# Optimization experiments

Hardware: AMD Instinct MI355X
Metric: run time of the kernel (lower is better)

The kernel has to match this reference:

```python
import jax, jax.numpy as jnp
import numpy as np
from jax import lax

DN = ('NCHW', 'OIHW', 'NCHW')

def conv(x, w, b):
    y = lax.conv_general_dilated(x, w, (1, 1), 'SAME', dimension_numbers=DN)
    return y + b[None, :, None, None]


def setup_inputs() -> dict:
    key = jax.random.key(0)
    ks = jax.random.split(key, 32)
    B, C, H, W = 16, 256, 40, 100
    dim, N, kd, ncls, mdim = 134, 4, 128, 2, 256
    inc = C + 2
    s = 0.05  # weight init scale
    def w(k, shape):
        return jax.random.normal(k, shape, jnp.float32) * s
    d = {}
    d['features'] = jax.random.normal(ks[0], (B, C, H, W), jnp.float32)
    d['iw0'] = w(ks[1], (dim, inc, 3, 3)); d['ib0'] = jnp.zeros((dim,), jnp.float32)
    d['iw1'] = w(ks[2], (dim, dim, 3, 3)); d['ib1'] = jnp.zeros((dim,), jnp.float32)
    d['iw2'] = w(ks[3], (dim, dim, 3, 3)); d['ib2'] = jnp.zeros((dim,), jnp.float32)
    d['iw3'] = w(ks[4], (dim, dim, 3, 3)); d['ib3'] = jnp.zeros((dim,), jnp.float32)
    d['iam_w'] = w(ks[5], (N, dim, 3, 3)); d['iam_b'] = jnp.zeros((N,), jnp.float32)
    d['cls_w'] = w(ks[6], (ncls, dim));    d['cls_b'] = jnp.zeros((ncls,), jnp.float32)
    d['mk_w'] = w(ks[7], (kd, dim));       d['mk_b'] = jnp.zeros((kd,), jnp.float32)
    d['mw0'] = w(ks[8], (mdim, inc, 3, 3));  d['mb0'] = jnp.zeros((mdim,), jnp.float32)
    d['mw1'] = w(ks[9], (mdim, mdim, 3, 3)); d['mb1'] = jnp.zeros((mdim,), jnp.float32)
    d['mw2'] = w(ks[10], (mdim, mdim, 3, 3)); d['mb2'] = jnp.zeros((mdim,), jnp.float32)
    d['mw3'] = w(ks[11], (mdim, mdim, 3, 3)); d['mb3'] = jnp.zeros((mdim,), jnp.float32)
    d['pw'] = w(ks[12], (kd, mdim, 1, 1));   d['pb'] = jnp.zeros((kd,), jnp.float32)
    return d


def reference(features, iw0, ib0, iw1, ib1, iw2, ib2, iw3, ib3, iam_w, iam_b,
              cls_w, cls_b, mk_w, mk_b, mw0, mb0, mw1, mb1, mw2, mb2, mw3, mb3, pw, pb):
    B, C, H, W = features.shape
    # coordinate channels in [-1, 1]
    y_loc = -1.0 + 2.0 * jnp.arange(H, dtype=jnp.float32) / (H - 1)
    x_loc = -1.0 + 2.0 * jnp.arange(W, dtype=jnp.float32) / (W - 1)
    yy, xx = jnp.meshgrid(y_loc, x_loc, indexing='ij')  # [H,W]
    coords = jnp.broadcast_to(jnp.stack([xx, yy], 0)[None], (B, 2, H, W))
    feat = jnp.concatenate([coords, features], axis=1)  # [B, C+2, H, W]

    # instance branch conv stack (258 -> 134, relu)
    f = jax.nn.relu(conv(feat, iw0, ib0))
    f = jax.nn.relu(conv(f, iw1, ib1))
    f = jax.nn.relu(conv(f, iw2, ib2))
    f = jax.nn.relu(conv(f, iw3, ib3))  # [B,134,H,W]

    params = jnp.transpose(f, (0, 2, 3, 1)).reshape(-1, 134)  # [B*H*W, 134]

    iam = conv(f, iam_w, iam_b)           # [B,N,H,W]
    iam_prob = jax.nn.sigmoid(iam)
    Bn, Ni = iam_prob.shape[:2]

    # seed extraction: per-map flat argmax (pos = r*W + c, label always 0 in original)
    pos = jnp.argmax(iam_prob.reshape(Bn * Ni, H * W), axis=-1)  # [B*N], values in [0, H*W)
    sel = params[pos]                     # gather rows (indexes batch-0 region, as in source)
    mask_params = sel[:, :67]
    reg_params = sel[:, 67:]

    # iam-weighted pooling
    ip = iam_prob.reshape(Bn, Ni, H * W)
    ip = ip / jnp.clip(ip.sum(-1, keepdims=True), 1e-6)
    inst = jnp.einsum('bnl,bcl->bnc', ip, f.reshape(Bn, 134, H * W))  # [B,N,134]

    pred_logits = inst @ cls_w.T + cls_b  # [B,N,2]
    pred_kernel = inst @ mk_w.T + mk_b    # [B,N,128]

    # mask branch (258 -> 256 x4 relu, then 1x1 projection to 128, no relu)
    m = jax.nn.relu(conv(feat, mw0, mb0))
    m = jax.nn.relu(conv(m, mw1, mb1))
    m = jax.nn.relu(conv(m, mw2, mb2))
    m = jax.nn.relu(conv(m, mw3, mb3))
    mf = conv(m, pw, pb)                  # [B,128,H,W]

    pred_masks = jnp.einsum('bnk,bkl->bnl', pred_kernel, mf.reshape(Bn, 128, H * W))
    pred_masks = pred_masks.reshape(Bn * Ni, H, W)
    pred_logits = pred_logits.reshape(Bn * Ni, -1)
    return pred_logits, mask_params, reg_params, pred_masks
```

## Files before the change

kernel.cpp:

```cpp
#include <hip/hip_runtime.h>
#include <hip/hip_bf16.h>
#include <math.h>

constexpr int HW = 4000;
constexpr int HP = 4284;
constexpr int HPAD = 4480;
constexpr int NPIXH = 16 * HP;

typedef short s16x8 __attribute__((ext_vector_type(8)));
typedef float f32x4 __attribute__((ext_vector_type(4)));
typedef unsigned short u16x4 __attribute__((ext_vector_type(4)));
typedef unsigned short u16;

__device__ __forceinline__ u16 f2bf(float f) {
    __hip_bfloat16 h = __float2bfloat16(f);
    u16 b; __builtin_memcpy(&b, &h, 2); return b;
}
__device__ __forceinline__ float bf2f(u16 b) {
    __hip_bfloat16 h; __builtin_memcpy(&h, &b, 2); return __bfloat162float(h);
}

__device__ __forceinline__ void gload_lds16(const void* g, void* l) {
    __builtin_amdgcn_global_load_lds(
        (const __attribute__((address_space(1))) void*)g,
        (__attribute__((address_space(3))) void*)l, 16, 0, 0);
}

__global__ __launch_bounds__(256) void repack_w(
    const float* __restrict__ W, u16* __restrict__ Wh, u16* __restrict__ Wl,
    int Cout, int Cin, int NRS, int nCh, int Npad, int do_lo)
{
    const int chunk = blockIdx.x * 256 + threadIdx.x;
    const int per = Npad * 4;
    const int total = NRS * nCh * per;
    if (chunk >= total) return;
    const int q = chunk % per;
    const int t2 = chunk / per;
    const int ch = t2 % nCh;
    const int rs = t2 / nCh;
    const int f = q >> 6, g = (q >> 4) & 3, rA = q & 15;
    const int n = f * 16 + rA;
    u16x4 hp[2], lp[2];
    #pragma unroll
    for (int j = 0; j < 8; ++j) {
        const int c = ch * 32 + g * 8 + j;
        const float v = (n < Cout && c < Cin) ? W[((size_t)n * Cin + c) * NRS + rs] : 0.f;
        const u16 hb = f2bf(v);
        hp[j >> 2][j & 3] = hb;
        lp[j >> 2][j & 3] = f2bf(v - bf2f(hb));
    }
    const size_t o = (size_t)chunk * 8;
    *(u16x4*)(Wh + o) = hp[0]; *(u16x4*)(Wh + o + 4) = hp[1];
    if (do_lo) { *(u16x4*)(Wl + o) = lp[0]; *(u16x4*)(Wl + o + 4) = lp[1]; }
}

__global__ __launch_bounds__(256) void prep_x0(
    const float* __restrict__ feat, u16* __restrict__ Xh, u16* __restrict__ Xl)
{
    const int p = blockIdx.x * 256 + threadIdx.x;
    if (p >= NPIXH) return;
    const int b = p / HP; const int rem = p - b * HP;
    const int hh = rem / 102, wp = rem - hh * 102;
    const bool halo = (hh == 0) | (hh == 41) | (wp == 0) | (wp == 101);
    const int h = hh - 1, w = wp - 1;
    const int hw = h * 100 + w;
    const float xw = -1.f + 2.f * (float)w / 99.f;
    const float yh = -1.f + 2.f * (float)h / 39.f;
    for (int g = 0; g < 36; ++g) {
        u16x4 hp[2], lp[2];
        #pragma unroll
        for (int j = 0; j < 8; ++j) {
            const int c = g * 8 + j;
            float v = 0.f;
            if (!halo) {
                if (c == 0) v = xw;
                else if (c == 1) v = yh;
                else if (c < 258) v = feat[((size_t)(b * 256 + (c - 2))) * HW + hw];
            }
            const u16 hb = f2bf(v);
            hp[j >> 2][j & 3] = hb;
            lp[j >> 2][j & 3] = f2bf(v - bf2f(hb));
        }
        const size_t o = ((size_t)(b * 36 + g) * HPAD + rem) * 8;
        *(u16x4*)(Xh + o) = hp[0]; *(u16x4*)(Xh + o + 4) = hp[1];
        *(u16x4*)(Xl + o) = lp[0]; *(u16x4*)(Xl + o + 4) = lp[1];
    }
}

__global__ __launch_bounds__(256) void zero_halo_pl(
    u16* __restrict__ pa, u16* __restrict__ pb, int nGa, int nGb)
{
    const int p = blockIdx.x * 256 + threadIdx.x;
    if (p >= NPIXH) return;
    const int b = p / HP; const int rem = p - b * HP;
    const int hh = rem / 102, wp = rem - hh * 102;
    if (!((hh == 0) | (hh == 41) | (wp == 0) | (wp == 101))) return;
    const u16x4 z = {0, 0, 0, 0};
    for (int g = 0; g < nGa; ++g) {
        const size_t o = ((size_t)(b * nGa + g) * HPAD + rem) * 8;
        *(u16x4*)(pa + o) = z; *(u16x4*)(pa + o + 4) = z;
    }
    if (pb)
        for (int g = 0; g < nGb; ++g) {
            const size_t o = ((size_t)(b * nGb + g) * HPAD + rem) * 8;
            *(u16x4*)(pb + o) = z; *(u16x4*)(pb + o + 4) = z;
        }
}

template <int SPLIT, int BN, int NRS, int OUTMODE, int NCH, int MINW>
__global__ __launch_bounds__(256, MINW) void conv_mfma(
    const u16* __restrict__ Xhi, const u16* __restrict__ Xlo,
    const u16* __restrict__ Whi, const u16* __restrict__ Wlo,
    const float* __restrict__ bias,
    u16* __restrict__ Yhi, u16* __restrict__ Ylo, float* __restrict__ Yf,
    int Npad, int Cout, int CoutStore, int nGout, int do_relu,
    int nN, int cpx)
{
    constexpr int FW = BN / 32;
    constexpr int PSTRIDE = 393;
    constexpr int NGIN = NCH * 4;
    constexpr int NPASS = (SPLIT == 3) ? 2 : 1;

    __shared__ u16 lsX[4 * PSTRIDE * 8];

    const int tid = threadIdx.x, lane = tid & 63, wid = tid >> 6;

    const int pb_ = blockIdx.x;
    const int s = (pb_ & 7) * cpx + (pb_ >> 3);
    const int nb = s % nN;
    const int mt = s / nN;
    const int mb = mt & 31, bimg = mt >> 5;
    const int off = mb * 128;
    const int n0 = nb * BN;
    const int h0 = off / 100, w0 = off - h0 * 100;
    const int pTL0 = h0 * 102 + w0;

    const int wn = (wid & 1) * (BN / 2);
    const int wm = (wid >> 1) * 64;
    const int gA = lane >> 4, rA = lane & 15;
    const int wq0 = ((n0 + wn) >> 4) * 64;

    int pd[4]; bool mval[4];
    #pragma unroll
    for (int fb = 0; fb < 4; ++fb) {
        int mm = off + wm + fb * 16 + rA;
        mval[fb] = mm < HW;
        if (!mval[fb]) mm = HW - 1;
        const int h = mm / 100, w = mm - h * 100;
        pd[fb] = (h * 102 + w) - pTL0;
    }

    auto stageX = [&](const u16* __restrict__ Xsrc, int ch) {
        const size_t src = ((size_t)(bimg * NGIN + ch * 4 + wid) * HPAD + pTL0) * 8;
        char* dst = (char*)lsX + wid * (PSTRIDE * 16);
        #pragma unroll
        for (int i = 0; i < 6; ++i)
            gload_lds16(Xsrc + src + (size_t)(i * 64 + lane) * 8, dst + i * 1024);
    };

    s16x8 wh[2][FW];
    s16x8 wl[2][SPLIT == 3 ? FW : 1];

    f32x4 acc[FW][4];
    #pragma unroll
    for (int i = 0; i < FW; ++i)
        #pragma unroll
        for (int j = 0; j < 4; ++j) acc[i][j] = (f32x4){0.f, 0.f, 0.f, 0.f};

    #pragma unroll
    for (int pass = 0; pass < NPASS; ++pass) {
        const u16* Xsrc = (NPASS == 2 && pass == 1) ? Xlo : Xhi;
        constexpr bool HASLO = (SPLIT == 3);
        const bool withLo = HASLO && (pass == 0);

        auto loadW = [&](int ch, int rs, int buf) {
            const size_t base = (((size_t)rs * NCH + ch) * (Npad * 4) + wq0 + lane) * 8;
            #pragma unroll
            for (int fa = 0; fa < FW; ++fa) {
                wh[buf][fa] = *(const s16x8*)(Whi + base + fa * 64 * 8);
                if constexpr (HASLO) {
                    if (withLo)
                        wl[buf][fa] = *(const s16x8*)(Wlo + base + fa * 64 * 8);
                }
            }
        };

        #pragma unroll 1
        for (int ch = 0; ch < NCH; ++ch) {
            if (ch | pass) __syncthreads();
            stageX(Xsrc, ch);
            loadW(ch, 0, 0);
            __syncthreads();

            #pragma unroll
            for (int rs = 0; rs < NRS; ++rs) {
                if (rs + 1 < NRS) loadW(ch, rs + 1, (rs + 1) & 1);
                const int toff = (NRS == 9) ? ((rs / 3) * 102 + (rs % 3)) : 103;

                s16x8 bX[4];
                #pragma unroll
                for (int fb = 0; fb < 4; ++fb) {
                    const int xi = (gA * PSTRIDE + pd[fb] + toff) * 8;
                    bX[fb] = *(const s16x8*)&lsX[xi];
                }
                #pragma unroll
                for (int fa = 0; fa < FW; ++fa)
                    #pragma unroll
                    for (int fb = 0; fb < 4; ++fb) {
                        acc[fa][fb] = __builtin_amdgcn_mfma_f32_16x16x32_bf16(
                            wh[rs & 1][fa], bX[fb], acc[fa][fb], 0, 0, 0);
                        if constexpr (HASLO) {
                            if (pass == 0)
                                acc[fa][fb] = __builtin_amdgcn_mfma_f32_16x16x32_bf16(
                                    wl[rs & 1][fa], bX[fb], acc[fa][fb], 0, 0, 0);
                        }
                    }
            }
        }
    }

    #pragma unroll
    for (int fb = 0; fb < 4; ++fb) {
        if (!mval[fb]) continue;
        const int mm = off + wm + fb * 16 + rA;
        #pragma unroll
        for (int fa = 0; fa < FW; ++fa) {
            const int nbc = n0 + wn + fa * 16 + gA * 4;
            if (nbc >= CoutStore) continue;
            f32x4 v = acc[fa][fb];
            #pragma unroll
            for (int i = 0; i < 4; ++i) {
                const int n = nbc + i;
                float x = (n < Cout) ? (v[i] + bias[n]) : 0.f;
                if (do_relu) x = fmaxf(x, 0.f);
                v[i] = x;
            }
            if constexpr (OUTMODE == 2) {
                *(f32x4*)(Yf + (size_t)(bimg * HW + mm) * CoutStore + nbc) = v;
            } else {
                const size_t o =
                    ((size_t)(bimg * nGout + (nbc >> 3)) * HPAD + pTL0 + pd[fb] + 103) * 8 + (nbc & 7);
                u16x4 hp;
                #pragma unroll
                for (int i = 0; i < 4; ++i) hp[i] = f2bf(v[i]);
                *(u16x4*)(Yhi + o) = hp;
                if constexpr (OUTMODE == 0) {
                    u16x4 lp;
                    #pragma unroll
                    for (int i = 0; i < 4; ++i) lp[i] = f2bf(v[i] - bf2f(hp[i]));
                    *(u16x4*)(Ylo + o) = lp;
                }
            }
        }
    }
}

__global__ __launch_bounds__(256) void iam_conv_nhwc(
    const u16* __restrict__ fhi, const u16* __restrict__ flo,
    const float* __restrict__ Wt, const float* __restrict__ bias,
    float* __restrict__ iam)
{
    __shared__ float wsm[9 * 134 * 4];
    const int tid = threadIdx.x;
    for (int i = tid; i < 4824; i += 256) {
        const int rs = i / 536; const int rem = i - rs * 536;
        const int c = rem >> 2; const int n = rem & 3;
        wsm[i] = Wt[(n * 134 + c) * 9 + rs];
    }
    __syncthreads();
    const int m = blockIdx.x * 256 + tid;
    const int b = m / HW; const int hw = m - b * HW;
    const int h = hw / 100, w = hw - h * 100;
    const int pTL = h * 102 + w;
    float a0 = bias[0], a1 = bias[1], a2 = bias[2], a3 = bias[3];
    for (int rs = 0; rs < 9; ++rs) {
        const int pA = pTL + (rs / 3) * 102 + (rs % 3);
        const float* wrow = &wsm[rs * 536];
        for (int g = 0; g < 17; ++g) {
            const size_t o = ((size_t)(b * 20 + g) * HPAD + pA) * 8;
            s16x8 hv = *(const s16x8*)(fhi + o);
            s16x8 lv = *(const s16x8*)(flo + o);
            #pragma unroll
            for (int j = 0; j < 8; ++j) {
                const int c = g * 8 + j;
                if (c < 134) {
                    const float v = bf2f((u16)hv[j]) + bf2f((u16)lv[j]);
                    const float* wc = wrow + c * 4;
                    a0 = fmaf(v, wc[0], a0); a1 = fmaf(v, wc[1], a1);
                    a2 = fmaf(v, wc[2], a2); a3 = fmaf(v, wc[3], a3);
                }
            }
        }
    }
    iam[(b * 4 + 0) * HW + hw] = a0;
    iam[(b * 4 + 1) * HW + hw] = a1;
    iam[(b * 4 + 2) * HW + hw] = a2;
    iam[(b * 4 + 3) * HW + hw] = a3;
}

__device__ __forceinline__ float sigmoidf_dev(float x) {
    return 1.f / (1.f + expf(-x));
}

__global__ __launch_bounds__(256) void stats_kernel(
    const float* __restrict__ iam, int* __restrict__ pos, float* __restrict__ denom)
{
    const int i = blockIdx.x;
    const int tid = threadIdx.x;
    const float* p = &iam[i * HW];
    float bm = -1e30f; int bi = 0; float sum = 0.f;
    for (int l = tid; l < HW; l += 256) {
        const float s = sigmoidf_dev(p[l]);
        sum += s;
        if (s > bm) { bm = s; bi = l; }
    }
    __shared__ float sm[256]; __shared__ int si[256]; __shared__ float ss[256];
    sm[tid] = bm; si[tid] = bi; ss[tid] = sum;
    __syncthreads();
    for (int off = 128; off > 0; off >>= 1) {
        if (tid < off) {
            ss[tid] += ss[tid + off];
            const float m2 = sm[tid + off]; const int i2 = si[tid + off];
            if (m2 > sm[tid] || (m2 == sm[tid] && i2 < si[tid])) { sm[tid] = m2; si[tid] = i2; }
        }
        __syncthreads();
    }
    if (tid == 0) { pos[i] = si[0]; denom[i] = fmaxf(ss[0], 1e-6f); }
}

__global__ __launch_bounds__(256) void inst_nhwc(
    const u16* __restrict__ fhi, const u16* __restrict__ flo,
    const float* __restrict__ iam, const float* __restrict__ denom,
    float* __restrict__ inst)
{
    const int b = blockIdx.x, g = blockIdx.y;
    const int tid = threadIdx.x;
    float acc[4][8] = {};
    const size_t pbase = (size_t)(b * 20 + g) * HPAD;
    for (int l = tid; l < HW; l += 256) {
        const int p = (l / 100 + 1) * 102 + (l % 100) + 1;
        s16x8 hv = *(const s16x8*)(fhi + (pbase + p) * 8);
        s16x8 lv = *(const s16x8*)(flo + (pbase + p) * 8);
        float fv[8];
        #pragma unroll
        for (int j = 0; j < 8; ++j) fv[j] = bf2f((u16)hv[j]) + bf2f((u16)lv[j]);
        #pragma unroll
        for (int n = 0; n < 4; ++n) {
            const float s = sigmoidf_dev(iam[(b * 4 + n) * HW + l]);
            #pragma unroll
            for (int j = 0; j < 8; ++j) acc[n][j] = fmaf(s, fv[j], acc[n][j]);
        }
    }
    __shared__ float red[128];
    const int lane = tid & 63, wid = tid >> 6;
    #pragma unroll
    for (int n = 0; n < 4; ++n)
        #pragma unroll
        for (int j = 0; j < 8; ++j) {
            float v = acc[n][j];
            #pragma unroll
            for (int off = 32; off > 0; off >>= 1) v += __shfl_xor(v, off);
            if (lane == 0) red[wid * 32 + n * 8 + j] = v;
        }
    __syncthreads();
    if (tid < 32) {
        const float s = red[tid] + red[32 + tid] + red[64 + tid] + red[96 + tid];
        const int n = tid >> 3, j = tid & 7;
        const int c = g * 8 + j;
        if (c < 134) inst[(b * 4 + n) * 134 + c] = s / denom[b * 4 + n];
    }
}

__global__ __launch_bounds__(128) void head_kernel(
    const float* __restrict__ inst,
    const float* __restrict__ cls_w, const float* __restrict__ cls_b,
    const float* __restrict__ mk_w, const float* __restrict__ mk_b,
    float* __restrict__ out_logits, float* __restrict__ pk)
{
    const int i = blockIdx.x;
    const int tid = threadIdx.x;
    __shared__ float iv[134];
    for (int c = tid; c < 134; c += 128) iv[c] = inst[i * 134 + c];
    __syncthreads();
    float a = mk_b[tid];
    for (int c = 0; c < 134; ++c) a = fmaf(iv[c], mk_w[tid * 134 + c], a);
    pk[i * 128 + tid] = a;
    if (tid < 2) {
        float g = cls_b[tid];
        for (int c = 0; c < 134; ++c) g = fmaf(iv[c], cls_w[tid * 134 + c], g);
        out_logits[i * 2 + tid] = g;
    }
}

__global__ void gather_nhwc(
    const u16* __restrict__ fhi, const u16* __restrict__ flo,
    const int* __restrict__ pos, float* __restrict__ outm, float* __restrict__ outr)
{
    const int i = blockIdx.x;
    const int c = threadIdx.x;
    if (c >= 134) return;
    const int p = pos[i];
    const int ph = (p / 100 + 1) * 102 + (p % 100) + 1;
    const size_t o = ((size_t)(c >> 3) * HPAD + ph) * 8 + (c & 7);
    const float v = bf2f(fhi[o]) + bf2f(flo[o]);
    if (c < 67) outm[i * 67 + c] = v;
    else        outr[i * 67 + (c - 67)] = v;
}

__global__ __launch_bounds__(256) void maskout_nhwc(
    const float* __restrict__ pk, const float* __restrict__ mf,
    float* __restrict__ outm)
{
    const int b = blockIdx.x, lc = blockIdx.y;
    const int tid = threadIdx.x;
    __shared__ float pks[4][128];
    for (int i = tid; i < 512; i += 256) pks[i >> 7][i & 127] = pk[b * 512 + i];
    __syncthreads();
    const int l = lc * 256 + tid;
    if (l >= HW) return;
    const float* row = mf + (size_t)(b * HW + l) * 128;
    float a[4] = {};
    for (int k = 0; k < 128; k += 4) {
        const f32x4 mv = *(const f32x4*)(row + k);
        #pragma unroll
        for (int n = 0; n < 4; ++n) {
            a[n] = fmaf(pks[n][k + 0], mv[0], a[n]);
            a[n] = fmaf(pks[n][k + 1], mv[1], a[n]);
            a[n] = fmaf(pks[n][k + 2], mv[2], a[n]);
            a[n] = fmaf(pks[n][k + 3], mv[3], a[n]);
        }
    }
    #pragma unroll
    for (int n = 0; n < 4; ++n) outm[(b * 4 + n) * HW + l] = a[n];
}

extern "C" void kernel_launch(void* const* d_in, const int* in_sizes, int n_in,
                              void* d_out, int out_size, void* d_ws, size_t ws_size,
                              hipStream_t stream)
{
    const float* features = (const float*)d_in[0];
    const float* iw0 = (const float*)d_in[1];
    const float* ib0 = (const float*)d_in[2];
    const float* iw1 = (const float*)d_in[3];
    const float* ib1 = (const float*)d_in[4];
    const float* iw2 = (const float*)d_in[5];
    const float* ib2 = (const float*)d_in[6];
    const float* iw3 = (const float*)d_in[7];
    const float* ib3 = (const float*)d_in[8];
    const float* iam_w = (const float*)d_in[9];
    const float* iam_b = (const float*)d_in[10];
    const float* cls_w = (const float*)d_in[11];
    const float* cls_b = (const float*)d_in[12];
    const float* mk_w = (const float*)d_in[13];
    const float* mk_b = (const float*)d_in[14];
    const float* mw0 = (const float*)d_in[15];
    const float* mb0 = (const float*)d_in[16];
    const float* mw1 = (const float*)d_in[17];
    const float* mb1 = (const float*)d_in[18];
    const float* mw2 = (const float*)d_in[19];
    const float* mb2 = (const float*)d_in[20];
    const float* mw3 = (const float*)d_in[21];
    const float* mb3 = (const float*)d_in[22];
    const float* pw = (const float*)d_in[23];
    const float* pb = (const float*)d_in[24];

    constexpr size_t WI0 = (size_t)9 * 9 * 160 * 4 * 16;
    constexpr size_t WI123 = (size_t)9 * 5 * 160 * 4 * 16;
    constexpr size_t WM0 = (size_t)9 * 9 * 256 * 4 * 16;
    constexpr size_t WM123 = (size_t)9 * 8 * 256 * 4 * 16;
    constexpr size_t WPJ = (size_t)1 * 8 * 128 * 4 * 16;
    constexpr size_t PLANE = (size_t)HPAD * 16;
    constexpr size_t X0SZ = (size_t)16 * 36 * PLANE;
    constexpr size_t P20 = (size_t)16 * 20 * PLANE;

    char* ws = (char*)d_ws;
    size_t off = 0;
    auto carve = [&](size_t bytes) { char* p = ws + off; off += (bytes + 255) & ~(size_t)255; return p; };
    u16* wi0h = (u16*)carve(WI0); u16* wi0l = (u16*)carve(WI0);
    u16* wi1h = (u16*)carve(WI123); u16* wi1l = (u16*)carve(WI123);
    u16* wi2h = (u16*)carve(WI123); u16* wi2l = (u16*)carve(WI123);
    u16* wi3h = (u16*)carve(WI123); u16* wi3l = (u16*)carve(WI123);
    u16* wm0h = (u16*)carve(WM0);
    u16* wm1h = (u16*)carve(WM123); u16* wm2h = (u16*)carve(WM123); u16* wm3h = (u16*)carve(WM123);
    u16* wpjh = (u16*)carve(WPJ);
    u16* X0hi = (u16*)carve(X0SZ);
    char* RGA = carve(X0SZ);
    char* RGB = carve(2 * P20);
    char* RGC = carve(2 * P20);
    float* iamb = (float*)carve(1024000);
    int* pos = (int*)carve(256);
    float* denom = (float*)carve(256);
    float* instb = (float*)carve(34560);
    float* pkbuf = (float*)carve(32768);

    u16* X0lo = (u16*)RGA;
    u16* MBhi = (u16*)RGA;
    u16* RAhi = (u16*)RGB; u16* RAlo = (u16*)(RGB + P20);
    u16* MAhi = (u16*)RGB;
    u16* RBhi = (u16*)RGC; u16* RBlo = (u16*)(RGC + P20);
    float* mf = (float*)RGC;

    float* out_logits = (float*)d_out;
    float* out_mask = out_logits + 128;
    float* out_reg = out_mask + 64 * 67;
    float* out_masks = out_reg + 64 * 67;

    const dim3 blk(256);
    auto rp = [&](const float* W, u16* h, u16* l, int Cout_, int Cin_, int NRS_,
                  int nCh_, int Npad_, int dolo) {
        const int tot = NRS_ * nCh_ * Npad_ * 4;
        repack_w<<<dim3((tot + 255) / 256), blk, 0, stream>>>(W, h, l, Cout_, Cin_, NRS_, nCh_, Npad_, dolo);
    };
    rp(iw0, wi0h, wi0l, 134, 258, 9, 9, 160, 1);
    rp(iw1, wi1h, wi1l, 134, 134, 9, 5, 160, 1);
    rp(iw2, wi2h, wi2l, 134, 134, 9, 5, 160, 1);
    rp(iw3, wi3h, wi3l, 134, 134, 9, 5, 160, 1);
    rp(mw0, wm0h, nullptr, 256, 258, 9, 9, 256, 0);
    rp(mw1, wm1h, nullptr, 256, 256, 9, 8, 256, 0);
    rp(mw2, wm2h, nullptr, 256, 256, 9, 8, 256, 0);
    rp(mw3, wm3h, nullptr, 256, 256, 9, 8, 256, 0);
    rp(pw, wpjh, nullptr, 128, 256, 1, 8, 128, 0);

    const dim3 gH((NPIXH + 255) / 256);
    prep_x0<<<gH, blk, 0, stream>>>(features, X0hi, X0lo);
    zero_halo_pl<<<gH, blk, 0, stream>>>(RAhi, RAlo, 20, 20);

    conv_mfma<3, 64, 9, 0, 9, 4><<<dim3(1536), blk, 0, stream>>>(
        X0hi, X0lo, wi0h, wi0l, ib0, RAhi, RAlo, nullptr, 160, 134, 160, 20, 1, 3, 192);
    zero_halo_pl<<<gH, blk, 0, stream>>>(RBhi, RBlo, 20, 20);
    conv_mfma<3, 64, 9, 0, 5, 4><<<dim3(1536), blk, 0, stream>>>(
        RAhi, RAlo, wi1h, wi1l, ib1, RBhi, RBlo, nullptr, 160, 134, 160, 20, 1, 3, 192);
    conv_mfma<3, 64, 9, 0, 5, 4><<<dim3(1536), blk, 0, stream>>>(
        RBhi, RBlo, wi2h, wi2l, ib2, RAhi, RAlo, nullptr, 160, 134, 160, 20, 1, 3, 192);
    conv_mfma<3, 64, 9, 0, 5, 4><<<dim3(1536), blk, 0, stream>>>(
        RAhi, RAlo, wi3h, wi3l, ib3, RBhi, RBlo, nullptr, 160, 134, 160, 20, 1, 3, 192);

    iam_conv_nhwc<<<dim3(250), blk, 0, stream>>>(RBhi, RBlo, iam_w, iam_b, iamb);
    stats_kernel<<<dim3(64), blk, 0, stream>>>(iamb, pos, denom);
    inst_nhwc<<<dim3(16, 17), blk, 0, stream>>>(RBhi, RBlo, iamb, denom, instb);
    head_kernel<<<dim3(64), dim3(128), 0, stream>>>(instb, cls_w, cls_b, mk_w, mk_b, out_logits, pkbuf);
    gather_nhwc<<<dim3(64), dim3(192), 0, stream>>>(RBhi, RBlo, pos, out_mask, out_reg);

    zero_halo_pl<<<gH, blk, 0, stream>>>(MAhi, MBhi, 32, 32);
    conv_mfma<1, 128, 9, 1, 9, 3><<<dim3(1024), blk, 0, stream>>>(
        X0hi, nullptr, wm0h, nullptr, mb0, MAhi, nullptr, nullptr, 256, 256, 256, 32, 1, 2, 128);
    conv_mfma<1, 128, 9, 1, 8, 3><<<dim3(1024), blk, 0, stream>>>(
        MAhi, nullptr, wm1h, nullptr, mb1, MBhi, nullptr, nullptr, 256, 256, 256, 32, 1, 2, 128);
    conv_mfma<1, 128, 9, 1, 8, 3><<<dim3(1024), blk, 0, stream>>>(
        MBhi, nullptr, wm2h, nullptr, mb2, MAhi, nullptr, nullptr, 256, 256, 256, 32, 1, 2, 128);
    conv_mfma<1, 128, 9, 1, 8, 3><<<dim3(1024), blk, 0, stream>>>(
        MAhi, nullptr, wm3h, nullptr, mb3, MBhi, nullptr, nullptr, 256, 256, 256, 32, 1, 2, 128);
    conv_mfma<1, 128, 1, 2, 8, 3><<<dim3(512), blk, 0, stream>>>(
        MBhi, nullptr, wpjh, nullptr, pb, nullptr, nullptr, mf, 128, 128, 128, 0, 0, 1, 64);

    maskout_nhwc<<<dim3(16, 16), blk, 0, stream>>>(pkbuf, mf, out_masks);
}
```

Before: 1.125 ms.

## Switch activation layout to 32-channel interleaved planes and retile instance convs

Activations move from 8-channel planes to 32-channel interleaved planes, so each pixel holds 64 contiguous bytes. Staging into LDS and the fragment reads change to match, and the padded LDS stride trick is dropped. Instance-branch convs now use 96-wide output tiles (Cout padded to 192, 1024 blocks), and the mask convs raise the occupancy hint from 3 to 4. The lo-weight loads are now issued per rs step, with the two MFMA passes split, which should cut register pressure. LDS bank conflicts may rise because the padding is gone, and the wider padding adds wasted compute on the instance branch.

After: 1.175 ms. 4.5% more time.

```diff
diff --git a/kernel.cpp b/kernel.cpp
--- a/kernel.cpp
+++ b/kernel.cpp
@@ -81,7 +81,7 @@
             hp[j >> 2][j & 3] = hb;
             lp[j >> 2][j & 3] = f2bf(v - bf2f(hb));
         }
-        const size_t o = ((size_t)(b * 36 + g) * HPAD + rem) * 8;
+        const size_t o = ((size_t)(b * 9 + (g >> 2)) * HPAD + rem) * 32 + (g & 3) * 8;
         *(u16x4*)(Xh + o) = hp[0]; *(u16x4*)(Xh + o + 4) = hp[1];
         *(u16x4*)(Xl + o) = lp[0]; *(u16x4*)(Xl + o + 4) = lp[1];
     }
@@ -97,13 +97,15 @@
     if (!((hh == 0) | (hh == 41) | (wp == 0) | (wp == 101))) return;
     const u16x4 z = {0, 0, 0, 0};
     for (int g = 0; g < nGa; ++g) {
-        const size_t o = ((size_t)(b * nGa + g) * HPAD + rem) * 8;
-        *(u16x4*)(pa + o) = z; *(u16x4*)(pa + o + 4) = z;
+        const size_t o = ((size_t)(b * nGa + g) * HPAD + rem) * 32;
+        #pragma unroll
+        for (int i = 0; i < 32; i += 4) *(u16x4*)(pa + o + i) = z;
     }
     if (pb)
         for (int g = 0; g < nGb; ++g) {
-            const size_t o = ((size_t)(b * nGb + g) * HPAD + rem) * 8;
-            *(u16x4*)(pb + o) = z; *(u16x4*)(pb + o + 4) = z;
+            const size_t o = ((size_t)(b * nGb + g) * HPAD + rem) * 32;
+            #pragma unroll
+            for (int i = 0; i < 32; i += 4) *(u16x4*)(pb + o + i) = z;
         }
 }
 
@@ -117,11 +119,10 @@
     int nN, int cpx)
 {
     constexpr int FW = BN / 32;
-    constexpr int PSTRIDE = 393;
-    constexpr int NGIN = NCH * 4;
     constexpr int NPASS = (SPLIT == 3) ? 2 : 1;
-
-    __shared__ u16 lsX[4 * PSTRIDE * 8];
+    constexpr bool HASLO = (SPLIT == 3);
+
+    __shared__ u16 lsX[384 * 32];
 
     const int tid = threadIdx.x, lane = tid & 63, wid = tid >> 6;
 
@@ -151,15 +152,21 @@
     }
 
     auto stageX = [&](const u16* __restrict__ Xsrc, int ch) {
-        const size_t src = ((size_t)(bimg * NGIN + ch * 4 + wid) * HPAD + pTL0) * 8;
-        char* dst = (char*)lsX + wid * (PSTRIDE * 16);
+        const size_t base = ((size_t)(bimg * NCH + ch) * HPAD + pTL0) * 32;
+        const int wo = wid * 6;
         #pragma unroll
         for (int i = 0; i < 6; ++i)
-            gload_lds16(Xsrc + src + (size_t)(i * 64 + lane) * 8, dst + i * 1024);
+            gload_lds16(Xsrc + base + (size_t)(wo + i) * 512 + lane * 8,
+                        (char*)lsX + (wo + i) * 1024);
     };
 
     s16x8 wh[2][FW];
-    s16x8 wl[2][SPLIT == 3 ? FW : 1];
+    auto loadWh = [&](int ch, int rs, int buf) {
+        const size_t b2 = (((size_t)rs * NCH + ch) * (Npad * 4) + wq0 + lane) * 8;
+        #pragma unroll
+        for (int fa = 0; fa < FW; ++fa)
+            wh[buf][fa] = *(const s16x8*)(Whi + b2 + fa * 64 * 8);
+    };
 
     f32x4 acc[FW][4];
     #pragma unroll
@@ -169,52 +176,45 @@
 
     #pragma unroll
     for (int pass = 0; pass < NPASS; ++pass) {
-        const u16* Xsrc = (NPASS == 2 && pass == 1) ? Xlo : Xhi;
-        constexpr bool HASLO = (SPLIT == 3);
-        const bool withLo = HASLO && (pass == 0);
-
-        auto loadW = [&](int ch, int rs, int buf) {
-            const size_t base = (((size_t)rs * NCH + ch) * (Npad * 4) + wq0 + lane) * 8;
-            #pragma unroll
-            for (int fa = 0; fa < FW; ++fa) {
-                wh[buf][fa] = *(const s16x8*)(Whi + base + fa * 64 * 8);
-                if constexpr (HASLO) {
-                    if (withLo)
-                        wl[buf][fa] = *(const s16x8*)(Wlo + base + fa * 64 * 8);
-                }
-            }
-        };
-
+        const u16* Xsrc = (HASLO && pass == 1) ? Xlo : Xhi;
         #pragma unroll 1
         for (int ch = 0; ch < NCH; ++ch) {
             if (ch | pass) __syncthreads();
             stageX(Xsrc, ch);
-            loadW(ch, 0, 0);
+            loadWh(ch, 0, 0);
             __syncthreads();
 
             #pragma unroll
             for (int rs = 0; rs < NRS; ++rs) {
-                if (rs + 1 < NRS) loadW(ch, rs + 1, (rs + 1) & 1);
+                if (rs + 1 < NRS) loadWh(ch, rs + 1, (rs + 1) & 1);
+                s16x8 wlc[HASLO ? FW : 1];
+                if (HASLO && pass == 0) {
+                    const size_t b2 = (((size_t)rs * NCH + ch) * (Npad * 4) + wq0 + lane) * 8;
+                    #pragma unroll
+                    for (int fa = 0; fa < FW; ++fa)
+                        wlc[fa] = *(const s16x8*)(Wlo + b2 + fa * 64 * 8);
+                }
                 const int toff = (NRS == 9) ? ((rs / 3) * 102 + (rs % 3)) : 103;
 
                 s16x8 bX[4];
                 #pragma unroll
-                for (int fb = 0; fb < 4; ++fb) {
-                    const int xi = (gA * PSTRIDE + pd[fb] + toff) * 8;
-                    bX[fb] = *(const s16x8*)&lsX[xi];
-                }
+                for (int fb = 0; fb < 4; ++fb)
+                    bX[fb] = *(const s16x8*)&lsX[(pd[fb] + toff) * 32 + gA * 8];
+
                 #pragma unroll
                 for (int fa = 0; fa < FW; ++fa)
                     #pragma unroll
-                    for (int fb = 0; fb < 4; ++fb) {
+                    for (int fb = 0; fb < 4; ++fb)
                         acc[fa][fb] = __builtin_amdgcn_mfma_f32_16x16x32_bf16(
                             wh[rs & 1][fa], bX[fb], acc[fa][fb], 0, 0, 0);
-                        if constexpr (HASLO) {
-                            if (pass == 0)
-                                acc[fa][fb] = __builtin_amdgcn_mfma_f32_16x16x32_bf16(
-                                    wl[rs & 1][fa], bX[fb], acc[fa][fb], 0, 0, 0);
-                        }
-                    }
+                if (HASLO && pass == 0) {
+                    #pragma unroll
+                    for (int fa = 0; fa < FW; ++fa)
+                        #pragma unroll
+                        for (int fb = 0; fb < 4; ++fb)
+                            acc[fa][fb] = __builtin_amdgcn_mfma_f32_16x16x32_bf16(
+                                wlc[fa], bX[fb], acc[fa][fb], 0, 0, 0);
+                }
             }
         }
     }
@@ -223,6 +223,7 @@
     for (int fb = 0; fb < 4; ++fb) {
         if (!mval[fb]) continue;
         const int mm = off + wm + fb * 16 + rA;
+        const int pix = pTL0 + pd[fb] + 103;
         #pragma unroll
         for (int fa = 0; fa < FW; ++fa) {
             const int nbc = n0 + wn + fa * 16 + gA * 4;
@@ -239,7 +240,7 @@
                 *(f32x4*)(Yf + (size_t)(bimg * HW + mm) * CoutStore + nbc) = v;
             } else {
                 const size_t o =
-                    ((size_t)(bimg * nGout + (nbc >> 3)) * HPAD + pTL0 + pd[fb] + 103) * 8 + (nbc & 7);
+                    ((size_t)(bimg * nGout + (nbc >> 5)) * HPAD + pix) * 32 + (nbc & 31);
                 u16x4 hp;
                 #pragma unroll
                 for (int i = 0; i < 4; ++i) hp[i] = f2bf(v[i]);
@@ -277,7 +278,7 @@
         const int pA = pTL + (rs / 3) * 102 + (rs % 3);
         const float* wrow = &wsm[rs * 536];
         for (int g = 0; g < 17; ++g) {
-            const size_t o = ((size_t)(b * 20 + g) * HPAD + pA) * 8;
+            const size_t o = ((size_t)(b * 5 + (g >> 2)) * HPAD + pA) * 32 + (g & 3) * 8;
             s16x8 hv = *(const s16x8*)(fhi + o);
             s16x8 lv = *(const s16x8*)(flo + o);
             #pragma unroll
@@ -336,11 +337,11 @@
     const int b = blockIdx.x, g = blockIdx.y;
     const int tid = threadIdx.x;
     float acc[4][8] = {};
-    const size_t pbase = (size_t)(b * 20 + g) * HPAD;
+    const size_t pbase = ((size_t)(b * 5 + (g >> 2)) * HPAD) * 32 + (g & 3) * 8;
     for (int l = tid; l < HW; l += 256) {
         const int p = (l / 100 + 1) * 102 + (l % 100) + 1;
-        s16x8 hv = *(const s16x8*)(fhi + (pbase + p) * 8);
-        s16x8 lv = *(const s16x8*)(flo + (pbase + p) * 8);
+        s16x8 hv = *(const s16x8*)(fhi + pbase + (size_t)p * 32);
+        s16x8 lv = *(const s16x8*)(flo + pbase + (size_t)p * 32);
         float fv[8];
         #pragma unroll
         for (int j = 0; j < 8; ++j) fv[j] = bf2f((u16)hv[j]) + bf2f((u16)lv[j]);
@@ -401,7 +402,7 @@
     if (c >= 134) return;
     const int p = pos[i];
     const int ph = (p / 100 + 1) * 102 + (p % 100) + 1;
-    const size_t o = ((size_t)(c >> 3) * HPAD + ph) * 8 + (c & 7);
+    const size_t o = ((size_t)(c >> 5) * HPAD + ph) * 32 + (c & 31);
     const float v = bf2f(fhi[o]) + bf2f(flo[o]);
     if (c < 67) outm[i * 67 + c] = v;
     else        outr[i * 67 + (c - 67)] = v;
@@ -464,14 +465,14 @@
     const float* pw = (const float*)d_in[23];
     const float* pb = (const float*)d_in[24];
 
-    constexpr size_t WI0 = (size_t)9 * 9 * 160 * 4 * 16;
-    constexpr size_t WI123 = (size_t)9 * 5 * 160 * 4 * 16;
+    constexpr size_t WI0 = (size_t)9 * 9 * 192 * 4 * 16;
+    constexpr size_t WI123 = (size_t)9 * 5 * 192 * 4 * 16;
     constexpr size_t WM0 = (size_t)9 * 9 * 256 * 4 * 16;
     constexpr size_t WM123 = (size_t)9 * 8 * 256 * 4 * 16;
     constexpr size_t WPJ = (size_t)1 * 8 * 128 * 4 * 16;
-    constexpr size_t PLANE = (size_t)HPAD * 16;
-    constexpr size_t X0SZ = (size_t)16 * 36 * PLANE;
-    constexpr size_t P20 = (size_t)16 * 20 * PLANE;
+    constexpr size_t CH32 = (size_t)HPAD * 64;
+    constexpr size_t X0SZ = (size_t)16 * 9 * CH32;
+    constexpr size_t PC5 = (size_t)16 * 5 * CH32;
 
     char* ws = (char*)d_ws;
     size_t off = 0;
@@ -485,8 +486,8 @@
     u16* wpjh = (u16*)carve(WPJ);
     u16* X0hi = (u16*)carve(X0SZ);
     char* RGA = carve(X0SZ);
-    char* RGB = carve(2 * P20);
-    char* RGC = carve(2 * P20);
+    char* RGB = carve(2 * PC5);
+    char* RGC = carve(2 * PC5);
     float* iamb = (float*)carve(1024000);
     int* pos = (int*)carve(256);
     float* denom = (float*)carve(256);
@@ -495,9 +496,9 @@
 
     u16* X0lo = (u16*)RGA;
     u16* MBhi = (u16*)RGA;
-    u16* RAhi = (u16*)RGB; u16* RAlo = (u16*)(RGB + P20);
+    u16* RAhi = (u16*)RGB; u16* RAlo = (u16*)(RGB + PC5);
     u16* MAhi = (u16*)RGB;
-    u16* RBhi = (u16*)RGC; u16* RBlo = (u16*)(RGC + P20);
+    u16* RBhi = (u16*)RGC; u16* RBlo = (u16*)(RGC + PC5);
     float* mf = (float*)RGC;
 
     float* out_logits = (float*)d_out;
@@ -511,10 +512,10 @@
         const int tot = NRS_ * nCh_ * Npad_ * 4;
         repack_w<<<dim3((tot + 255) / 256), blk, 0, stream>>>(W, h, l, Cout_, Cin_, NRS_, nCh_, Npad_, dolo);
     };
-    rp(iw0, wi0h, wi0l, 134, 258, 9, 9, 160, 1);
-    rp(iw1, wi1h, wi1l, 134, 134, 9, 5, 160, 1);
-    rp(iw2, wi2h, wi2l, 134, 134, 9, 5, 160, 1);
-    rp(iw3, wi3h, wi3l, 134, 134, 9, 5, 160, 1);
+    rp(iw0, wi0h, wi0l, 134, 258, 9, 9, 192, 1);
+    rp(iw1, wi1h, wi1l, 134, 134, 9, 5, 192, 1);
+    rp(iw2, wi2h, wi2l, 134, 134, 9, 5, 192, 1);
+    rp(iw3, wi3h, wi3l, 134, 134, 9, 5, 192, 1);
     rp(mw0, wm0h, nullptr, 256, 258, 9, 9, 256, 0);
     rp(mw1, wm1h, nullptr, 256, 256, 9, 8, 256, 0);
     rp(mw2, wm2h, nullptr, 256, 256, 9, 8, 256, 0);
@@ -523,17 +524,17 @@
 
     const dim3 gH((NPIXH + 255) / 256);
     prep_x0<<<gH, blk, 0, stream>>>(features, X0hi, X0lo);
-    zero_halo_pl<<<gH, blk, 0, stream>>>(RAhi, RAlo, 20, 20);
-
-    conv_mfma<3, 64, 9, 0, 9, 4><<<dim3(1536), blk, 0, stream>>>(
-        X0hi, X0lo, wi0h, wi0l, ib0, RAhi, RAlo, nullptr, 160, 134, 160, 20, 1, 3, 192);
-    zero_halo_pl<<<gH, blk, 0, stream>>>(RBhi, RBlo, 20, 20);
-    conv_mfma<3, 64, 9, 0, 5, 4><<<dim3(1536), blk, 0, stream>>>(
-        RAhi, RAlo, wi1h, wi1l, ib1, RBhi, RBlo, nullptr, 160, 134, 160, 20, 1, 3, 192);
-    conv_mfma<3, 64, 9, 0, 5, 4><<<dim3(1536), blk, 0, stream>>>(
-        RBhi, RBlo, wi2h, wi2l, ib2, RAhi, RAlo, nullptr, 160, 134, 160, 20, 1, 3, 192);
-    conv_mfma<3, 64, 9, 0, 5, 4><<<dim3(1536), blk, 0, stream>>>(
-        RAhi, RAlo, wi3h, wi3l, ib3, RBhi, RBlo, nullptr, 160, 134, 160, 20, 1, 3, 192);
+    zero_halo_pl<<<gH, blk, 0, stream>>>(RAhi, RAlo, 5, 5);
+
+    conv_mfma<3, 96, 9, 0, 9, 4><<<dim3(1024), blk, 0, stream>>>(
+        X0hi, X0lo, wi0h, wi0l, ib0, RAhi, RAlo, nullptr, 192, 134, 160, 5, 1, 2, 128);
+    zero_halo_pl<<<gH, blk, 0, stream>>>(RBhi, RBlo, 5, 5);
+    conv_mfma<3, 96, 9, 0, 5, 4><<<dim3(1024), blk, 0, stream>>>(
+        RAhi, RAlo, wi1h, wi1l, ib1, RBhi, RBlo, nullptr, 192, 134, 160, 5, 1, 2, 128);
+    conv_mfma<3, 96, 9, 0, 5, 4><<<dim3(1024), blk, 0, stream>>>(
+        RBhi, RBlo, wi2h, wi2l, ib2, RAhi, RAlo, nullptr, 192, 134, 160, 5, 1, 2, 128);
+    conv_mfma<3, 96, 9, 0, 5, 4><<<dim3(1024), blk, 0, stream>>>(
+        RAhi, RAlo, wi3h, wi3l, ib3, RBhi, RBlo, nullptr, 192, 134, 160, 5, 1, 2, 128);
 
     iam_conv_nhwc<<<dim3(250), blk, 0, stream>>>(RBhi, RBlo, iam_w, iam_b, iamb);
     stats_kernel<<<dim3(64), blk, 0, stream>>>(iamb, pos, denom);
@@ -541,16 +542,16 @@
     head_kernel<<<dim3(64), dim3(128), 0, stream>>>(instb, cls_w, cls_b, mk_w, mk_b, out_logits, pkbuf);
     gather_nhwc<<<dim3(64), dim3(192), 0, stream>>>(RBhi, RBlo, pos, out_mask, out_reg);
 
-    zero_halo_pl<<<gH, blk, 0, stream>>>(MAhi, MBhi, 32, 32);
-    conv_mfma<1, 128, 9, 1, 9, 3><<<dim3(1024), blk, 0, stream>>>(
-        X0hi, nullptr, wm0h, nullptr, mb0, MAhi, nullptr, nullptr, 256, 256, 256, 32, 1, 2, 128);
-    conv_mfma<1, 128, 9, 1, 8, 3><<<dim3(1024), blk, 0, stream>>>(
-        MAhi, nullptr, wm1h, nullptr, mb1, MBhi, nullptr, nullptr, 256, 256, 256, 32, 1, 2, 128);
-    conv_mfma<1, 128, 9, 1, 8, 3><<<dim3(1024), blk, 0, stream>>>(
-        MBhi, nullptr, wm2h, nullptr, mb2, MAhi, nullptr, nullptr, 256, 256, 256, 32, 1, 2, 128);
-    conv_mfma<1, 128, 9, 1, 8, 3><<<dim3(1024), blk, 0, stream>>>(
-        MAhi, nullptr, wm3h, nullptr, mb3, MBhi, nullptr, nullptr, 256, 256, 256, 32, 1, 2, 128);
-    conv_mfma<1, 128, 1, 2, 8, 3><<<dim3(512), blk, 0, stream>>>(
+    zero_halo_pl<<<gH, blk, 0, stream>>>(MAhi, MBhi, 8, 8);
+    conv_mfma<1, 128, 9, 1, 9, 4><<<dim3(1024), blk, 0, stream>>>(
+        X0hi, nullptr, wm0h, nullptr, mb0, MAhi, nullptr, nullptr, 256, 256, 256, 8, 1, 2, 128);
+    conv_mfma<1, 128, 9, 1, 8, 4><<<dim3(1024), blk, 0, stream>>>(
+        MAhi, nullptr, wm1h, nullptr, mb1, MBhi, nullptr, nullptr, 256, 256, 256, 8, 1, 2, 128);
+    conv_mfma<1, 128, 9, 1, 8, 4><<<dim3(1024), blk, 0, stream>>>(
+        MBhi, nullptr, wm2h, nullptr, mb2, MAhi, nullptr, nullptr, 256, 256, 256, 8, 1, 2, 128);
+    conv_mfma<1, 128, 9, 1, 8, 4><<<dim3(1024), blk, 0, stream>>>(
+        MAhi, nullptr, wm3h, nullptr, mb3, MBhi, nullptr, nullptr, 256, 256, 256, 8, 1, 2, 128);
+    conv_mfma<1, 128, 1, 2, 8, 4><<<dim3(512), blk, 0, stream>>>(
         MBhi, nullptr, wpjh, nullptr, pb, nullptr, nullptr, mf, 128, 128, 128, 0, 0, 1, 64);
 
     maskout_nhwc<<<dim3(16, 16), blk, 0, stream>>>(pkbuf, mf, out_masks);
```
